# Kernel tuning notes

Hardware: AMD Instinct MI355X
Metric: run time of the kernel (lower is better)

## Reference

```python
import jax, jax.numpy as jnp
import numpy as np

WIN = (7, 7)
NUM_HEADS = 6
DIM = 192
NW = 64          # windows per image
BATCH = 64       # images
B_ = BATCH * NW  # 4096 window-batches
N = WIN[0] * WIN[1]  # 49


def _relative_position_index():
    ch, cw = np.arange(WIN[0]), np.arange(WIN[1])
    coords = np.stack(np.meshgrid(ch, cw, indexing='ij'))          # [2, Wh, Ww]
    cf = coords.reshape(2, -1)                                      # [2, N]
    rel = cf[:, :, None] - cf[:, None, :]                           # [2, N, N]
    rel = rel.transpose(1, 2, 0).astype(np.int64)                   # [N, N, 2]
    rel[:, :, 0] += WIN[0] - 1
    rel[:, :, 1] += WIN[1] - 1
    rel[:, :, 0] *= 2 * WIN[1] - 1
    return rel.sum(-1).astype(np.int32)                             # [N, N]


def setup_inputs() -> dict:
    key = jax.random.key(0)
    ks = jax.random.split(key, 8)
    x = jax.random.normal(ks[0], (B_, N, DIM), dtype=jnp.float32)
    # additive shift-window mask: 0 where allowed, -100 where disallowed
    u = jax.random.uniform(ks[1], (NW, N, N))
    attn_mask = jnp.where(u < 0.15, -100.0, 0.0).astype(jnp.float32)
    rpb_table = jax.random.normal(ks[2], ((2 * WIN[0] - 1) * (2 * WIN[1] - 1), NUM_HEADS), dtype=jnp.float32) * 0.02
    rel_index = jnp.asarray(_relative_position_index())
    std = 1.0 / np.sqrt(DIM)
    qkv_w = jax.random.normal(ks[3], (3 * DIM, DIM), dtype=jnp.float32) * std
    qkv_b = jax.random.normal(ks[4], (3 * DIM,), dtype=jnp.float32) * 0.02
    proj_w = jax.random.normal(ks[5], (DIM, DIM), dtype=jnp.float32) * std
    proj_b = jax.random.normal(ks[6], (DIM,), dtype=jnp.float32) * 0.02
    return {"x": x, "attn_mask": attn_mask, "rpb_table": rpb_table,
            "rel_index": rel_index, "qkv_w": qkv_w, "qkv_b": qkv_b,
            "proj_w": proj_w, "proj_b": proj_b}


def reference(x, attn_mask, rpb_table, rel_index, qkv_w, qkv_b, proj_w, proj_b):
    Bw, n, C = x.shape
    H = NUM_HEADS
    hd = C // H
    scale = hd ** -0.5
    # qkv projection: [Bw, N, 3, H, hd] -> (3, Bw, H, N, hd)
    qkv = (x @ qkv_w.T + qkv_b).reshape(Bw, n, 3, H, hd).transpose(2, 0, 3, 1, 4)
    q, k, v = qkv[0], qkv[1], qkv[2]
    # gathered relative position bias: [H, N, N]
    rel_bias = rpb_table[rel_index.reshape(-1)].reshape(n, n, H).transpose(2, 0, 1)
    # scores [Bw, H, N, N]
    attn = jnp.einsum('bhnd,bhmd->bhnm', q * scale, k) + rel_bias[None]
    nW = attn_mask.shape[0]
    attn = attn.reshape(Bw // nW, nW, H, n, n) + attn_mask[None, :, None]
    attn = jax.nn.softmax(attn.reshape(Bw, H, n, n), axis=-1)
    out = jnp.einsum('bhnm,bhmd->bhnd', attn, v)  # [Bw, H, N, hd]
    out = out.transpose(0, 2, 1, 3).reshape(Bw, n, C)
    return out @ proj_w.T + proj_b
```

## Files before the change

### kernel.cpp

```cpp
#include <hip/hip_runtime.h>
#include <stdint.h>

typedef unsigned short ushort_t;
typedef __attribute__((ext_vector_type(8))) short bf16x8;
typedef __attribute__((ext_vector_type(4))) float f32x4;
typedef __attribute__((ext_vector_type(4))) unsigned int u32x4;

#define NTOK 49
#define DIMC 192
#define NH 6
#define HD 32
#define SCALE 0.17677669529663687f
#define XS 200
#define VTS 72
#define PS 72
#define MS 66
#define RS 68

#define OFF_X    0
#define OFF_Q    25600
#define OFF_K    51200
#define OFF_VT   76800
#define OFF_P    104448
#define OFF_MASK 122880
#define OFF_RPB  139776
#define OFF_REL  145184
#define OFF_BQ   153888
#define OFF_BP   156192
#define SMEM_BYTES 156960

#define QKVW_N (576 * 192)
#define PROJW_N (192 * 192)
#define QKV_GRP (4 * 9 * 6 * 64)
#define PROJ_GRP (4 * 3 * 6 * 64)
#define WBF_BYTES ((QKVW_N + PROJW_N) * 2)
#define BIAS_FLOATS (64 * 6 * 4 * 4 * 4 * 16 * 4)
#define WS_NEED1 ((size_t)WBF_BYTES)
#define WS_NEED2 ((size_t)WBF_BYTES + (size_t)BIAS_FLOATS * 4)

__device__ __forceinline__ ushort_t f2bf(float f) {
    uint32_t x = __builtin_bit_cast(uint32_t, f);
    x += 0x7fffu + ((x >> 16) & 1u);
    return (ushort_t)(x >> 16);
}
__device__ __forceinline__ uint32_t cvtpk(float lo, float hi) {
    uint32_t r;
    asm("v_cvt_pk_bf16_f32 %0, %1, %2" : "=v"(r) : "v"(lo), "v"(hi));
    return r;
}

__device__ __forceinline__ bf16x8 cvt8(const float* p) {
    f32x4 a = *(const f32x4*)p;
    f32x4 b = *(const f32x4*)(p + 4);
    bf16x8 r;
    r[0] = (short)f2bf(a[0]); r[1] = (short)f2bf(a[1]);
    r[2] = (short)f2bf(a[2]); r[3] = (short)f2bf(a[3]);
    r[4] = (short)f2bf(b[0]); r[5] = (short)f2bf(b[1]);
    r[6] = (short)f2bf(b[2]); r[7] = (short)f2bf(b[3]);
    return r;
}

__global__ __launch_bounds__(256) void swz_weights_kernel(
    const float* __restrict__ qkvw, const float* __restrict__ projw,
    ushort_t* __restrict__ dst)
{
    int i = blockIdx.x * 256 + threadIdx.x;
    if (i >= QKV_GRP + PROJ_GRP) return;
    const float* src;
    float s = 1.0f;
    if (i < QKV_GRP) {
        int lane = i & 63, t = i >> 6;
        int kk = t % 6, nt = (t / 6) % 9, cq = t / 54;
        int col = cq * 144 + nt * 16 + (lane & 15);
        int k0 = kk * 32 + (lane >> 4) * 8;
        src = qkvw + col * DIMC + k0;
        if (col < 192) s = SCALE;
    } else {
        int j = i - QKV_GRP;
        int lane = j & 63, t = j >> 6;
        int kk = t % 6, nt = (t / 6) % 3, cq = t / 18;
        int col = cq * 48 + nt * 16 + (lane & 15);
        int k0 = kk * 32 + (lane >> 4) * 8;
        src = projw + col * DIMC + k0;
    }
    f32x4 a = *(const f32x4*)src;
    f32x4 b = *(const f32x4*)(src + 4);
    u32x4 o;
    o[0] = (uint32_t)f2bf(a[0] * s) | ((uint32_t)f2bf(a[1] * s) << 16);
    o[1] = (uint32_t)f2bf(a[2] * s) | ((uint32_t)f2bf(a[3] * s) << 16);
    o[2] = (uint32_t)f2bf(b[0] * s) | ((uint32_t)f2bf(b[1] * s) << 16);
    o[3] = (uint32_t)f2bf(b[2] * s) | ((uint32_t)f2bf(b[3] * s) << 16);
    *(u32x4*)(dst + (size_t)i * 8) = o;
}

__global__ __launch_bounds__(256) void bias_kernel(
    const float* __restrict__ mask_g, const float* __restrict__ rpb_g,
    const int* __restrict__ rel_g, float* __restrict__ dst)
{
    int i = blockIdx.x * 256 + threadIdx.x;
    if (i >= BIAS_FLOATS / 4) return;
    int c = i & 15, g = (i >> 4) & 3, t = (i >> 6) & 3, wsid = (i >> 8) & 3;
    int hw = i >> 10;
    int h = hw % 6, wi = hw / 6;
    int m0 = 16 * wsid + 4 * g, n = 16 * t + c;
    f32x4 v;
    #pragma unroll
    for (int r = 0; r < 4; ++r) {
        int m = m0 + r;
        float val;
        if (n >= NTOK)      val = -30000.0f;
        else if (m >= NTOK) val = 0.0f;
        else val = mask_g[(size_t)wi * (NTOK * NTOK) + m * NTOK + n]
                 + rpb_g[(size_t)rel_g[m * NTOK + n] * NH + h];
        v[r] = val;
    }
    *(f32x4*)(dst + (size_t)i * 4) = v;
}

template <int MODE>
__global__ __launch_bounds__(512, 2) void win_attn_kernel(
    const float* __restrict__ x_g,
    const float* __restrict__ mask_g,
    const float* __restrict__ rpb_g,
    const int* __restrict__ rel_g,
    const float* __restrict__ qkvw_g,
    const float* __restrict__ qkvb_g,
    const float* __restrict__ projw_g,
    const float* __restrict__ projb_g,
    const ushort_t* __restrict__ wbf_g,
    const float* __restrict__ bias_g,
    float* __restrict__ out_g)
{
    extern __shared__ char smem[];
    ushort_t* x_lds  = (ushort_t*)(smem + OFF_X);
    ushort_t* q_lds  = (ushort_t*)(smem + OFF_Q);
    ushort_t* k_lds  = (ushort_t*)(smem + OFF_K);
    ushort_t* vT     = (ushort_t*)(smem + OFF_VT);
    ushort_t* P_lds  = (ushort_t*)(smem + OFF_P);
    float*    mask_p = (float*)(smem + OFF_MASK);
    float*    rpb_l  = (float*)(smem + OFF_RPB);
    ushort_t* rel_p  = (ushort_t*)(smem + OFF_REL);
    float*    bq     = (float*)(smem + OFF_BQ);
    float*    bp     = (float*)(smem + OFF_BP);

    const int tid  = threadIdx.x;
    const int b    = blockIdx.x;
    const int wi   = b & 63;
    const int w    = tid >> 6;
    const int lane = tid & 63;
    const int g    = lane >> 4;
    const int c    = lane & 15;

    {
        const float* xg = x_g + (size_t)b * (NTOK * DIMC);
        for (int i = tid; i < 64 * 24; i += 512) {
            int row = i / 24, col = (i % 24) * 8;
            u32x4 v = {0u, 0u, 0u, 0u};
            if (row < NTOK) {
                const float* src = xg + row * DIMC + col;
                f32x4 a = *(const f32x4*)src;
                f32x4 d = *(const f32x4*)(src + 4);
                v[0] = cvtpk(a[0], a[1]); v[1] = cvtpk(a[2], a[3]);
                v[2] = cvtpk(d[0], d[1]); v[3] = cvtpk(d[2], d[3]);
            }
            *(u32x4*)&x_lds[row * XS + col] = v;
        }
        if constexpr (MODE < 2) {
            const float* mw = mask_g + (size_t)wi * (NTOK * NTOK);
            for (int i = tid; i < 64 * 64; i += 512) {
                int m = i >> 6, n = i & 63;
                float f;
                if (n >= NTOK)      f = -30000.0f;
                else if (m >= NTOK) f = 0.0f;
                else                f = mw[m * NTOK + n];
                mask_p[m * MS + n] = f;
                rel_p[m * RS + n] = (m < NTOK && n < NTOK) ? (ushort_t)rel_g[m * NTOK + n]
                                                           : (ushort_t)0;
            }
            for (int i = tid; i < 169 * 6; i += 512)
                rpb_l[(i / 6) * 8 + (i % 6)] = rpb_g[i];
        }
        for (int i = tid; i < 576; i += 512) {
            float v = qkvb_g[i];
            if constexpr (MODE >= 1) { if (i < 192) v *= SCALE; }
            bq[i] = v;
        }
        if (tid < 192) bp[tid] = projb_g[tid];
    }
    __syncthreads();

    {
        const int mh = w >> 2, cq = w & 3;
        const ushort_t* wq = wbf_g + (size_t)cq * (9 * 6 * 64 * 8);

        bf16x8 ring[4][6];
        if constexpr (MODE >= 1) {
            #pragma unroll
            for (int p = 0; p < 3; ++p)
                #pragma unroll
                for (int kk = 0; kk < 6; ++kk)
                    ring[p][kk] = *(const bf16x8*)(wq + (size_t)((p * 6 + kk) * 64 + lane) * 8);
            __builtin_amdgcn_sched_barrier(0);
        }

        bf16x8 ax[2][6];
        #pragma unroll
        for (int mt = 0; mt < 2; ++mt)
            #pragma unroll
            for (int kk = 0; kk < 6; ++kk)
                ax[mt][kk] = *(const bf16x8*)&x_lds[(32 * mh + 16 * mt + c) * XS + kk * 32 + g * 8];

        #pragma unroll
        for (int nt = 0; nt < 9; ++nt) {
            const int cg = 144 * cq + nt * 16 + c;
            bf16x8 bw[6];
            if constexpr (MODE >= 1) {
                if (nt + 3 < 9) {
                    #pragma unroll
                    for (int kk = 0; kk < 6; ++kk)
                        ring[(nt + 3) & 3][kk] =
                            *(const bf16x8*)(wq + (size_t)(((nt + 3) * 6 + kk) * 64 + lane) * 8);
                }
                __builtin_amdgcn_sched_barrier(0);
                #pragma unroll
                for (int kk = 0; kk < 6; ++kk) bw[kk] = ring[nt & 3][kk];
            } else {
                #pragma unroll
                for (int kk = 0; kk < 6; ++kk)
                    bw[kk] = cvt8(qkvw_g + (size_t)cg * DIMC + kk * 32 + g * 8);
            }
            const float bias = bq[cg];
            f32x4 acc[2];
            acc[0] = (f32x4){bias, bias, bias, bias};
            acc[1] = acc[0];
            #pragma unroll
            for (int kk = 0; kk < 6; ++kk)
                #pragma unroll
                for (int mt = 0; mt < 2; ++mt)
                    acc[mt] = __builtin_amdgcn_mfma_f32_16x16x32_bf16(ax[mt][kk], bw[kk], acc[mt], 0, 0, 0);

            const int seg = 144 * cq + nt * 16;
            if (seg < 192) {
                #pragma unroll
                for (int mt = 0; mt < 2; ++mt) {
                    uint32_t p01 = cvtpk(acc[mt][0], acc[mt][1]);
                    uint32_t p23 = cvtpk(acc[mt][2], acc[mt][3]);
                    const int r0 = 32 * mh + 16 * mt + g * 4;
                    q_lds[(r0 + 0) * XS + cg] = (ushort_t)p01;
                    q_lds[(r0 + 1) * XS + cg] = (ushort_t)(p01 >> 16);
                    q_lds[(r0 + 2) * XS + cg] = (ushort_t)p23;
                    q_lds[(r0 + 3) * XS + cg] = (ushort_t)(p23 >> 16);
                }
            } else if (seg < 384) {
                const int ck = cg - 192;
                #pragma unroll
                for (int mt = 0; mt < 2; ++mt) {
                    uint32_t p01 = cvtpk(acc[mt][0], acc[mt][1]);
                    uint32_t p23 = cvtpk(acc[mt][2], acc[mt][3]);
                    const int r0 = 32 * mh + 16 * mt + g * 4;
                    k_lds[(r0 + 0) * XS + ck] = (ushort_t)p01;
                    k_lds[(r0 + 1) * XS + ck] = (ushort_t)(p01 >> 16);
                    k_lds[(r0 + 2) * XS + ck] = (ushort_t)p23;
                    k_lds[(r0 + 3) * XS + ck] = (ushort_t)(p23 >> 16);
                }
            } else {
                const int cv = cg - 384;
                #pragma unroll
                for (int mt = 0; mt < 2; ++mt) {
                    uint32_t* dst = (uint32_t*)&vT[cv * VTS + 32 * mh + 16 * mt + g * 4];
                    dst[0] = cvtpk(acc[mt][0], acc[mt][1]);
                    dst[1] = cvtpk(acc[mt][2], acc[mt][3]);
                }
            }
        }
    }
    __syncthreads();

    bf16x8 pw[3][6];
    {
        const int wsid = w & 3, hh = w >> 2;
        ushort_t* Pw = P_lds + w * (16 * PS);
        const int mq0 = 16 * wsid + g * 4;

        auto head = [&](int h) {
            bf16x8 aq = *(const bf16x8*)&q_lds[(16 * wsid + c) * XS + h * HD + g * 8];
            f32x4 S[4];
            if constexpr (MODE == 2) {
                const float* bC = bias_g + ((size_t)((wi * 6 + h) * 4 + wsid) * 4) * 256 + lane * 4;
                #pragma unroll
                for (int t = 0; t < 4; ++t) {
                    f32x4 Ct = *(const f32x4*)(bC + t * 256);
                    bf16x8 bk = *(const bf16x8*)&k_lds[(16 * t + c) * XS + h * HD + g * 8];
                    S[t] = __builtin_amdgcn_mfma_f32_16x16x32_bf16(aq, bk, Ct, 0, 0, 0);
                }
            } else {
                #pragma unroll
                for (int t = 0; t < 4; ++t) {
                    bf16x8 bk = *(const bf16x8*)&k_lds[(16 * t + c) * XS + h * HD + g * 8];
                    f32x4 z = {0.f, 0.f, 0.f, 0.f};
                    S[t] = __builtin_amdgcn_mfma_f32_16x16x32_bf16(aq, bk, z, 0, 0, 0);
                }
            }
            float rinv[4];
            #pragma unroll
            for (int r = 0; r < 4; ++r) {
                float sv[4];
                if constexpr (MODE == 2) {
                    #pragma unroll
                    for (int t = 0; t < 4; ++t) sv[t] = S[t][r];
                } else {
                    const int mq = mq0 + r;
                    const float*    mrow = mask_p + mq * MS;
                    const ushort_t* rrow = rel_p + mq * RS;
                    #pragma unroll
                    for (int t = 0; t < 4; ++t) {
                        const int n = 16 * t + c;
                        float sc = (MODE == 0) ? SCALE : 1.0f;
                        sv[t] = S[t][r] * sc + rpb_l[(int)rrow[n] * 8 + h] + mrow[n];
                    }
                }
                float vmax = fmaxf(fmaxf(sv[0], sv[1]), fmaxf(sv[2], sv[3]));
                #pragma unroll
                for (int xm = 1; xm < 16; xm <<= 1)
                    vmax = fmaxf(vmax, __shfl_xor(vmax, xm));
                float sum = 0.f;
                float ev[4];
                #pragma unroll
                for (int t = 0; t < 4; ++t) {
                    ev[t] = __expf(fmaxf(sv[t] - vmax, -80.0f));
                    sum += ev[t];
                }
                #pragma unroll
                for (int xm = 1; xm < 16; xm <<= 1)
                    sum += __shfl_xor(sum, xm);
                rinv[r] = 1.0f / sum;
                uint32_t p01 = cvtpk(ev[0], ev[1]);
                uint32_t p23 = cvtpk(ev[2], ev[3]);
                ushort_t* pr = Pw + (g * 4 + r) * PS + c;
                pr[0]  = (ushort_t)p01;
                pr[16] = (ushort_t)(p01 >> 16);
                pr[32] = (ushort_t)p23;
                pr[48] = (ushort_t)(p23 >> 16);
            }
            f32x4 z = {0.f, 0.f, 0.f, 0.f};
            f32x4 O[2] = {z, z};
            #pragma unroll
            for (int ks = 0; ks < 2; ++ks) {
                bf16x8 ap = *(const bf16x8*)&Pw[c * PS + ks * 32 + g * 8];
                #pragma unroll
                for (int nt = 0; nt < 2; ++nt) {
                    bf16x8 bv = *(const bf16x8*)&vT[(h * HD + nt * 16 + c) * VTS + ks * 32 + g * 8];
                    O[nt] = __builtin_amdgcn_mfma_f32_16x16x32_bf16(ap, bv, O[nt], 0, 0, 0);
                }
            }
            #pragma unroll
            for (int r = 0; r < 4; ++r) {
                uint32_t po = cvtpk(O[0][r] * rinv[r], O[1][r] * rinv[r]);
                ushort_t* ar = x_lds + (16 * wsid + g * 4 + r) * XS + h * HD + c;
                ar[0]  = (ushort_t)po;
                ar[16] = (ushort_t)(po >> 16);
            }
        };

        head(hh * 3 + 0);
        head(hh * 3 + 1);
        if constexpr (MODE >= 1) {
            const int cq4 = w & 3;
            const ushort_t* wp = wbf_g + QKVW_N + (size_t)cq4 * (3 * 6 * 64 * 8);
            #pragma unroll
            for (int nt = 0; nt < 3; ++nt)
                #pragma unroll
                for (int kk = 0; kk < 6; ++kk)
                    pw[nt][kk] = *(const bf16x8*)(wp + (size_t)((nt * 6 + kk) * 64 + lane) * 8);
            __builtin_amdgcn_sched_barrier(0);
        }
        head(hh * 3 + 2);
    }
    __syncthreads();

    {
        const int mh = w >> 2, cq4 = w & 3;
        bf16x8 aa[2][6];
        #pragma unroll
        for (int mt = 0; mt < 2; ++mt)
            #pragma unroll
            for (int kk = 0; kk < 6; ++kk)
                aa[mt][kk] = *(const bf16x8*)&x_lds[(32 * mh + 16 * mt + c) * XS + kk * 32 + g * 8];

        float* og = out_g + (size_t)b * (NTOK * DIMC);
        #pragma unroll
        for (int nt = 0; nt < 3; ++nt) {
            const int cg = 48 * cq4 + nt * 16 + c;
            bf16x8 bw[6];
            #pragma unroll
            for (int kk = 0; kk < 6; ++kk) {
                if constexpr (MODE >= 1)
                    bw[kk] = pw[nt][kk];
                else
                    bw[kk] = cvt8(projw_g + (size_t)cg * DIMC + kk * 32 + g * 8);
            }
            const float bias = bp[cg];
            f32x4 acc[2];
            acc[0] = (f32x4){bias, bias, bias, bias};
            acc[1] = acc[0];
            #pragma unroll
            for (int kk = 0; kk < 6; ++kk)
                #pragma unroll
                for (int mt = 0; mt < 2; ++mt)
                    acc[mt] = __builtin_amdgcn_mfma_f32_16x16x32_bf16(aa[mt][kk], bw[kk], acc[mt], 0, 0, 0);
            #pragma unroll
            for (int mt = 0; mt < 2; ++mt)
                #pragma unroll
                for (int r = 0; r < 4; ++r) {
                    const int row = 32 * mh + 16 * mt + g * 4 + r;
                    if (row < NTOK) og[row * DIMC + cg] = acc[mt][r];
                }
        }
    }
}

extern "C" void kernel_launch(void* const* d_in, const int* in_sizes, int n_in,
                              void* d_out, int out_size, void* d_ws, size_t ws_size,
                              hipStream_t stream) {
    (void)in_sizes; (void)n_in; (void)out_size;
    const float* x_g     = (const float*)d_in[0];
    const float* mask_g  = (const float*)d_in[1];
    const float* rpb_g   = (const float*)d_in[2];
    const int*   rel_g   = (const int*)d_in[3];
    const float* qkvw_g  = (const float*)d_in[4];
    const float* qkvb_g  = (const float*)d_in[5];
    const float* projw_g = (const float*)d_in[6];
    const float* projb_g = (const float*)d_in[7];
    float*       out_g   = (float*)d_out;

    const bool has_w = (d_ws != nullptr) && (ws_size >= WS_NEED1);
    const bool has_b = (d_ws != nullptr) && (ws_size >= WS_NEED2);
    ushort_t* wbf = (ushort_t*)d_ws;
    float* bias4 = (float*)((char*)d_ws + WBF_BYTES);

    if (has_w) {
        int ngrp = QKV_GRP + PROJ_GRP;
        hipLaunchKernelGGL(swz_weights_kernel, dim3((ngrp + 255) / 256), dim3(256), 0, stream,
                           qkvw_g, projw_g, wbf);
    }
    if (has_b) {
        int nthr = BIAS_FLOATS / 4;
        hipLaunchKernelGGL(bias_kernel, dim3((nthr + 255) / 256), dim3(256), 0, stream,
                           mask_g, rpb_g, rel_g, bias4);
        hipFuncSetAttribute((const void*)win_attn_kernel<2>,
                            hipFuncAttributeMaxDynamicSharedMemorySize, SMEM_BYTES);
        hipLaunchKernelGGL(win_attn_kernel<2>, dim3(4096), dim3(512), SMEM_BYTES, stream,
                           x_g, mask_g, rpb_g, rel_g, qkvw_g, qkvb_g, projw_g, projb_g,
                           wbf, bias4, out_g);
    } else if (has_w) {
        hipFuncSetAttribute((const void*)win_attn_kernel<1>,
                            hipFuncAttributeMaxDynamicSharedMemorySize, SMEM_BYTES);
        hipLaunchKernelGGL(win_attn_kernel<1>, dim3(4096), dim3(512), SMEM_BYTES, stream,
                           x_g, mask_g, rpb_g, rel_g, qkvw_g, qkvb_g, projw_g, projb_g,
                           wbf, (const float*)nullptr, out_g);
    } else {
        hipFuncSetAttribute((const void*)win_attn_kernel<0>,
                            hipFuncAttributeMaxDynamicSharedMemorySize, SMEM_BYTES);
        hipLaunchKernelGGL(win_attn_kernel<0>, dim3(4096), dim3(512), SMEM_BYTES, stream,
                           x_g, mask_g, rpb_g, rel_g, qkvw_g, qkvb_g, projw_g, projb_g,
                           (const ushort_t*)nullptr, (const float*)nullptr, out_g);
    }
}
```

Baseline: 237.7 us.

## Interleave per-head QK^T, softmax and PV stages and drop softmax max reduction

In the precomputed-bias path (MODE 2), the per-head attention is split into separate QK^T, softmax and PV stages. These are interleaved across the three heads each wave handles, so the next head's MFMAs can overlap the current head's exp and shuffle work. The MFMA sections are wrapped in s_setprio raises to favour matrix issue. The softmax also drops the row-max subtraction, its shuffle reduction and the clamp, exponentiating raw scores directly. That saves a reduction per row but can overflow if scores are ever large, and the interleaving keeps more score registers live at once.

```diff
diff --git a/kernel.cpp b/kernel.cpp
--- a/kernel.cpp
+++ b/kernel.cpp
@@ -282,99 +282,163 @@
         ushort_t* Pw = P_lds + w * (16 * PS);
         const int mq0 = 16 * wsid + g * 4;
 
-        auto head = [&](int h) {
-            bf16x8 aq = *(const bf16x8*)&q_lds[(16 * wsid + c) * XS + h * HD + g * 8];
-            f32x4 S[4];
-            if constexpr (MODE == 2) {
+        if constexpr (MODE == 2) {
+            const int h0 = hh * 3;
+            float rinv0[4], rinv1[4], rinv2[4];
+            f32x4 S0[4], S1[4], S2[4];
+
+            auto QKT = [&](int h, f32x4* S) {
+                bf16x8 aq = *(const bf16x8*)&q_lds[(16 * wsid + c) * XS + h * HD + g * 8];
                 const float* bC = bias_g + ((size_t)((wi * 6 + h) * 4 + wsid) * 4) * 256 + lane * 4;
+                __builtin_amdgcn_s_setprio(1);
                 #pragma unroll
                 for (int t = 0; t < 4; ++t) {
                     f32x4 Ct = *(const f32x4*)(bC + t * 256);
                     bf16x8 bk = *(const bf16x8*)&k_lds[(16 * t + c) * XS + h * HD + g * 8];
                     S[t] = __builtin_amdgcn_mfma_f32_16x16x32_bf16(aq, bk, Ct, 0, 0, 0);
                 }
-            } else {
+                __builtin_amdgcn_s_setprio(0);
+            };
+            auto SM = [&](f32x4* S, float* rinv) {
+                #pragma unroll
+                for (int r = 0; r < 4; ++r) {
+                    float e0 = __expf(S[0][r]), e1 = __expf(S[1][r]);
+                    float e2 = __expf(S[2][r]), e3 = __expf(S[3][r]);
+                    float sum = (e0 + e1) + (e2 + e3);
+                    #pragma unroll
+                    for (int xm = 1; xm < 16; xm <<= 1)
+                        sum += __shfl_xor(sum, xm);
+                    rinv[r] = 1.0f / sum;
+                    uint32_t p01 = cvtpk(e0, e1);
+                    uint32_t p23 = cvtpk(e2, e3);
+                    ushort_t* pr = Pw + (g * 4 + r) * PS + c;
+                    pr[0]  = (ushort_t)p01;
+                    pr[16] = (ushort_t)(p01 >> 16);
+                    pr[32] = (ushort_t)p23;
+                    pr[48] = (ushort_t)(p23 >> 16);
+                }
+            };
+            auto PV = [&](int h, const float* rinv) {
+                f32x4 z = {0.f, 0.f, 0.f, 0.f};
+                f32x4 O[2] = {z, z};
+                __builtin_amdgcn_s_setprio(1);
+                #pragma unroll
+                for (int ks = 0; ks < 2; ++ks) {
+                    bf16x8 ap = *(const bf16x8*)&Pw[c * PS + ks * 32 + g * 8];
+                    #pragma unroll
+                    for (int nt = 0; nt < 2; ++nt) {
+                        bf16x8 bv = *(const bf16x8*)&vT[(h * HD + nt * 16 + c) * VTS + ks * 32 + g * 8];
+                        O[nt] = __builtin_amdgcn_mfma_f32_16x16x32_bf16(ap, bv, O[nt], 0, 0, 0);
+                    }
+                }
+                __builtin_amdgcn_s_setprio(0);
+                #pragma unroll
+                for (int r = 0; r < 4; ++r) {
+                    uint32_t po = cvtpk(O[0][r] * rinv[r], O[1][r] * rinv[r]);
+                    ushort_t* ar = x_lds + (16 * wsid + g * 4 + r) * XS + h * HD + c;
+                    ar[0]  = (ushort_t)po;
+                    ar[16] = (ushort_t)(po >> 16);
+                }
+            };
+
+            QKT(h0 + 0, S0);
+            QKT(h0 + 1, S1);
+            SM(S0, rinv0);
+            QKT(h0 + 2, S2);
+            PV(h0 + 0, rinv0);
+            SM(S1, rinv1);
+            PV(h0 + 1, rinv1);
+            {
+                const int cq4 = w & 3;
+                const ushort_t* wp = wbf_g + QKVW_N + (size_t)cq4 * (3 * 6 * 64 * 8);
+                #pragma unroll
+                for (int nt = 0; nt < 3; ++nt)
+                    #pragma unroll
+                    for (int kk = 0; kk < 6; ++kk)
+                        pw[nt][kk] = *(const bf16x8*)(wp + (size_t)((nt * 6 + kk) * 64 + lane) * 8);
+                __builtin_amdgcn_sched_barrier(0);
+            }
+            SM(S2, rinv2);
+            PV(h0 + 2, rinv2);
+        } else {
+            auto head = [&](int h) {
+                bf16x8 aq = *(const bf16x8*)&q_lds[(16 * wsid + c) * XS + h * HD + g * 8];
+                f32x4 S[4];
                 #pragma unroll
                 for (int t = 0; t < 4; ++t) {
                     bf16x8 bk = *(const bf16x8*)&k_lds[(16 * t + c) * XS + h * HD + g * 8];
                     f32x4 z = {0.f, 0.f, 0.f, 0.f};
                     S[t] = __builtin_amdgcn_mfma_f32_16x16x32_bf16(aq, bk, z, 0, 0, 0);
                 }
-            }
-            float rinv[4];
-            #pragma unroll
-            for (int r = 0; r < 4; ++r) {
-                float sv[4];
-                if constexpr (MODE == 2) {
-                    #pragma unroll
-                    for (int t = 0; t < 4; ++t) sv[t] = S[t][r];
-                } else {
+                float rinv[4];
+                #pragma unroll
+                for (int r = 0; r < 4; ++r) {
                     const int mq = mq0 + r;
                     const float*    mrow = mask_p + mq * MS;
                     const ushort_t* rrow = rel_p + mq * RS;
+                    float sv[4];
                     #pragma unroll
                     for (int t = 0; t < 4; ++t) {
                         const int n = 16 * t + c;
                         float sc = (MODE == 0) ? SCALE : 1.0f;
                         sv[t] = S[t][r] * sc + rpb_l[(int)rrow[n] * 8 + h] + mrow[n];
                     }
-                }
-                float vmax = fmaxf(fmaxf(sv[0], sv[1]), fmaxf(sv[2], sv[3]));
-                #pragma unroll
-                for (int xm = 1; xm < 16; xm <<= 1)
-                    vmax = fmaxf(vmax, __shfl_xor(vmax, xm));
-                float sum = 0.f;
-                float ev[4];
-                #pragma unroll
-                for (int t = 0; t < 4; ++t) {
-                    ev[t] = __expf(fmaxf(sv[t] - vmax, -80.0f));
-                    sum += ev[t];
-                }
-                #pragma unroll
-                for (int xm = 1; xm < 16; xm <<= 1)
-                    sum += __shfl_xor(sum, xm);
-                rinv[r] = 1.0f / sum;
-                uint32_t p01 = cvtpk(ev[0], ev[1]);
-                uint32_t p23 = cvtpk(ev[2], ev[3]);
-                ushort_t* pr = Pw + (g * 4 + r) * PS + c;
-                pr[0]  = (ushort_t)p01;
-                pr[16] = (ushort_t)(p01 >> 16);
-                pr[32] = (ushort_t)p23;
-                pr[48] = (ushort_t)(p23 >> 16);
-            }
-            f32x4 z = {0.f, 0.f, 0.f, 0.f};
-            f32x4 O[2] = {z, z};
-            #pragma unroll
-            for (int ks = 0; ks < 2; ++ks) {
-                bf16x8 ap = *(const bf16x8*)&Pw[c * PS + ks * 32 + g * 8];
-                #pragma unroll
-                for (int nt = 0; nt < 2; ++nt) {
-                    bf16x8 bv = *(const bf16x8*)&vT[(h * HD + nt * 16 + c) * VTS + ks * 32 + g * 8];
-                    O[nt] = __builtin_amdgcn_mfma_f32_16x16x32_bf16(ap, bv, O[nt], 0, 0, 0);
-                }
-            }
-            #pragma unroll
-            for (int r = 0; r < 4; ++r) {
-                uint32_t po = cvtpk(O[0][r] * rinv[r], O[1][r] * rinv[r]);
-                ushort_t* ar = x_lds + (16 * wsid + g * 4 + r) * XS + h * HD + c;
-                ar[0]  = (ushort_t)po;
-                ar[16] = (ushort_t)(po >> 16);
-            }
-        };
-
-        head(hh * 3 + 0);
-        head(hh * 3 + 1);
-        if constexpr (MODE >= 1) {
-            const int cq4 = w & 3;
-            const ushort_t* wp = wbf_g + QKVW_N + (size_t)cq4 * (3 * 6 * 64 * 8);
-            #pragma unroll
-            for (int nt = 0; nt < 3; ++nt)
-                #pragma unroll
-                for (int kk = 0; kk < 6; ++kk)
-                    pw[nt][kk] = *(const bf16x8*)(wp + (size_t)((nt * 6 + kk) * 64 + lane) * 8);
-            __builtin_amdgcn_sched_barrier(0);
-        }
-        head(hh * 3 + 2);
+                    float vmax = fmaxf(fmaxf(sv[0], sv[1]), fmaxf(sv[2], sv[3]));
+                    #pragma unroll
+                    for (int xm = 1; xm < 16; xm <<= 1)
+                        vmax = fmaxf(vmax, __shfl_xor(vmax, xm));
+                    float sum = 0.f;
+                    float ev[4];
+                    #pragma unroll
+                    for (int t = 0; t < 4; ++t) {
+                        ev[t] = __expf(fmaxf(sv[t] - vmax, -80.0f));
+                        sum += ev[t];
+                    }
+                    #pragma unroll
+                    for (int xm = 1; xm < 16; xm <<= 1)
+                        sum += __shfl_xor(sum, xm);
+                    rinv[r] = 1.0f / sum;
+                    uint32_t p01 = cvtpk(ev[0], ev[1]);
+                    uint32_t p23 = cvtpk(ev[2], ev[3]);
+                    ushort_t* pr = Pw + (g * 4 + r) * PS + c;
+                    pr[0]  = (ushort_t)p01;
+                    pr[16] = (ushort_t)(p01 >> 16);
+                    pr[32] = (ushort_t)p23;
+                    pr[48] = (ushort_t)(p23 >> 16);
+                }
+                f32x4 z = {0.f, 0.f, 0.f, 0.f};
+                f32x4 O[2] = {z, z};
+                #pragma unroll
+                for (int ks = 0; ks < 2; ++ks) {
+                    bf16x8 ap = *(const bf16x8*)&Pw[c * PS + ks * 32 + g * 8];
+                    #pragma unroll
+                    for (int nt = 0; nt < 2; ++nt) {
+                        bf16x8 bv = *(const bf16x8*)&vT[(h * HD + nt * 16 + c) * VTS + ks * 32 + g * 8];
+                        O[nt] = __builtin_amdgcn_mfma_f32_16x16x32_bf16(ap, bv, O[nt], 0, 0, 0);
+                    }
+                }
+                #pragma unroll
+                for (int r = 0; r < 4; ++r) {
+                    uint32_t po = cvtpk(O[0][r] * rinv[r], O[1][r] * rinv[r]);
+                    ushort_t* ar = x_lds + (16 * wsid + g * 4 + r) * XS + h * HD + c;
+                    ar[0]  = (ushort_t)po;
+                    ar[16] = (ushort_t)(po >> 16);
+                }
+            };
+            head(hh * 3 + 0);
+            head(hh * 3 + 1);
+            if constexpr (MODE >= 1) {
+                const int cq4 = w & 3;
+                const ushort_t* wp = wbf_g + QKVW_N + (size_t)cq4 * (3 * 6 * 64 * 8);
+                #pragma unroll
+                for (int nt = 0; nt < 3; ++nt)
+                    #pragma unroll
+                    for (int kk = 0; kk < 6; ++kk)
+                        pw[nt][kk] = *(const bf16x8*)(wp + (size_t)((nt * 6 + kk) * 64 + lane) * 8);
+                __builtin_amdgcn_sched_barrier(0);
+            }
+            head(hh * 3 + 2);
+        }
     }
     __syncthreads();
 
```

Result: faster. 221.3 us (-6.9%).
